# Kernel tuning notes

Hardware: AMD Instinct MI355X
Metric: run time of the kernel (lower is better)

## Reference

```python
import jax, jax.numpy as jnp
import numpy as np

L, N, C = 8192, 8, 3
DIM, DIM_OUT, K, RATIO = 64, 128, 16, 0.25
L2 = int(L * RATIO)  # 2048; note L % L2 == 0 (needed for the fmod quirk)
EPS = 1e-5


def layer_norm(x, g, b):
    m = jnp.mean(x, axis=-1, keepdims=True)
    v = jnp.mean(jnp.square(x - m), axis=-1, keepdims=True)  # biased var, as torch LayerNorm
    return (x - m) * jax.lax.rsqrt(v + EPS) * g + b


def mlp(x, w1, g1, b1, w2, g2, b2):
    h = x @ w1.T
    h = layer_norm(h, g1, b1)
    h = h @ w2.T
    h = layer_norm(h, g2, b2)
    return jax.nn.relu(h)


def setup_inputs() -> dict:
    key = jax.random.key(0)
    ks = jax.random.split(key, 5)
    coords = jax.random.normal(ks[0], (L, N, C), jnp.float32)
    features = jax.random.normal(ks[1], (L, N, DIM), jnp.float32)
    s1 = 1.0 / np.sqrt(DIM)
    s2 = 1.0 / np.sqrt(DIM_OUT)
    w1 = jax.random.uniform(ks[2], (DIM_OUT, DIM), jnp.float32, -s1, s1)
    w2 = jax.random.uniform(ks[3], (DIM_OUT, DIM_OUT), jnp.float32, -s2, s2)
    g1 = jnp.ones((DIM_OUT,), jnp.float32)
    b1 = jnp.zeros((DIM_OUT,), jnp.float32)
    g2 = jnp.ones((DIM_OUT,), jnp.float32)
    b2 = jnp.zeros((DIM_OUT,), jnp.float32)
    # RandomDecimate: random permutation of point indices, keep first L2 (same across batch)
    keep_idx = jax.random.permutation(ks[4], L)[:L2].astype(jnp.int32)
    return dict(coords=coords, features=features, w1=w1, g1=g1, b1=b1,
                w2=w2, g2=g2, b2=b2, keep_idx=keep_idx)


def reference(coords, features, w1, g1, b1, w2, g2, b2, keep_idx):
    # MLP on all points: [L, N, DIM_OUT]
    feats = mlp(features, w1, g1, b1, w2, g2, b2)
    # decimation: keep_coords [L2, N, C]
    keep_coords = coords[keep_idx]
    # per-batch KNN of kept points against all points
    c = coords.transpose(1, 0, 2)        # [N, L, C]
    kc = keep_coords.transpose(1, 0, 2)  # [N, L2, C]
    d2 = (jnp.sum(kc * kc, -1)[:, :, None]
          + jnp.sum(c * c, -1)[:, None, :]
          - 2.0 * jnp.einsum('nic,njc->nij', kc, c))  # [N, L2, L]
    _, nn_idx = jax.lax.top_k(-d2, K)    # [N, L2, K] indices into [0, L)
    # faithful to clusters.fmod_(L2) on flattened idx n*L+l (L % L2 == 0 => l % L2)
    nn_idx = nn_idx % L2
    # fused gather + amax pooling over K neighbors
    fT = feats.transpose(1, 0, 2)  # [N, L, DIM_OUT]
    gathered = jax.vmap(lambda f, idx: f[idx])(fT, nn_idx)  # [N, L2, K, DIM_OUT]
    pool_features = jnp.max(gathered, axis=2).transpose(1, 0, 2)  # [L2, N, DIM_OUT]
    return keep_coords, pool_features
```

## Files before the change

kernel.cpp:

```cpp
#include <hip/hip_runtime.h>
#include <stdint.h>

#define L_    8192
#define N_    8
#define L2_   2048
#define K_    16

typedef unsigned int uint;
typedef unsigned short ushort;
typedef unsigned long long u64;
typedef __attribute__((ext_vector_type(8))) short bh8;
typedef __attribute__((ext_vector_type(4))) float f32x4;

__device__ __forceinline__ ushort f2b(float f){
  uint u = __float_as_uint(f);
  return (ushort)((u + 0x7FFFu + ((u >> 16) & 1u)) >> 16);
}
__device__ __forceinline__ uint ford(float f){
  uint u = __float_as_uint(f);
  return u ^ ((uint)((int)u >> 31) | 0x80000000u);
}
__device__ __forceinline__ float unford(uint u){
  uint v = (u & 0x80000000u) ? (u ^ 0x80000000u) : ~u;
  return __uint_as_float(v);
}

__device__ __forceinline__ void ld8(float* t, const float* p){
  float4 a = *(const float4*)p; float4 b = *(const float4*)(p + 4);
  t[0]=a.x; t[1]=a.y; t[2]=a.z; t[3]=a.w; t[4]=b.x; t[5]=b.y; t[6]=b.z; t[7]=b.w;
}
__device__ __forceinline__ bh8 pack8(const float* v){
  bh8 r;
  #pragma unroll
  for (int j = 0; j < 8; ++j) r[j] = (short)f2b(v[j]);
  return r;
}

__global__ __launch_bounds__(256) void prep_pack_k(const float* __restrict__ coords,
                                                   const int* __restrict__ keep,
                                                   const float* __restrict__ w1,
                                                   const float* __restrict__ w2,
                                                   float* __restrict__ out0,
                                                   ushort* __restrict__ pw1,
                                                   ushort* __restrict__ pw2,
                                                   float4* __restrict__ sCF,
                                                   uint* __restrict__ oIdx,
                                                   uint* __restrict__ sPos,
                                                   float4* __restrict__ cBB){
  int blk = blockIdx.x;
  int tid = threadIdx.x;
  if (blk < 96){
    int e = blk * 256 + tid;
    if (e < 8192) pw1[e] = f2b(w1[e]);
    else          pw2[e - 8192] = f2b(w2[e - 8192]);
    return;
  }
  if (blk < 288){
    int t = (blk - 96) * 256 + tid;
    int i = t / 24; int rem = t - i * 24;
    out0[t] = coords[(size_t)keep[i] * 24 + rem];
    return;
  }
  int n = blk - 288;
  __shared__ uint hist[4096];
  __shared__ uint wsum[4];
  int lane = tid & 63, wv = tid >> 6;
  for (int i = tid; i < 4096; i += 256) hist[i] = 0;
  __syncthreads();
  for (int t = tid; t < 8192; t += 256){
    const float* cr = coords + ((size_t)t * 8 + n) * 3;
    float x = cr[0], y = cr[1], z = cr[2];
    int ix = (int)floorf((x + 4.f) * 2.f); ix = ix < 0 ? 0 : (ix > 15 ? 15 : ix);
    int iy = (int)floorf((y + 4.f) * 2.f); iy = iy < 0 ? 0 : (iy > 15 ? 15 : iy);
    int iz = (int)floorf((z + 4.f) * 2.f); iz = iz < 0 ? 0 : (iz > 15 ? 15 : iz);
    atomicAdd(&hist[(ix << 8) | (iy << 4) | iz], 1u);
  }
  __syncthreads();
  uint tt = 0;
  #pragma unroll
  for (int j = 0; j < 16; ++j) tt += hist[tid * 16 + j];
  uint sc = tt;
  #pragma unroll
  for (int m = 1; m < 64; m <<= 1){
    uint o = __shfl_up(sc, m, 64);
    if (lane >= m) sc += o;
  }
  if (lane == 63) wsum[wv] = sc;
  __syncthreads();
  uint wbase = 0;
  for (int w = 0; w < wv; ++w) wbase += wsum[w];
  uint run = wbase + sc - tt;
  #pragma unroll
  for (int j = 0; j < 16; ++j){
    uint v = hist[tid * 16 + j];
    hist[tid * 16 + j] = run;
    run += v;
  }
  __syncthreads();
  for (int t = tid; t < 8192; t += 256){
    const float* cr = coords + ((size_t)t * 8 + n) * 3;
    float x = cr[0], y = cr[1], z = cr[2];
    float cc;
    {
      #pragma clang fp contract(off)
      cc = x*x + y*y + z*z;
    }
    int ix = (int)floorf((x + 4.f) * 2.f); ix = ix < 0 ? 0 : (ix > 15 ? 15 : ix);
    int iy = (int)floorf((y + 4.f) * 2.f); iy = iy < 0 ? 0 : (iy > 15 ? 15 : iy);
    int iz = (int)floorf((z + 4.f) * 2.f); iz = iz < 0 ? 0 : (iz > 15 ? 15 : iz);
    uint pos = atomicAdd(&hist[(ix << 8) | (iy << 4) | iz], 1u);
    sCF[(n << 13) + pos] = make_float4(x, y, z, cc);
    oIdx[(n << 13) + pos] = (uint)t;
    sPos[(n << 13) + t]   = pos;
  }
  __syncthreads();
  if (tid < 128){
    float4 mn = make_float4(3.4e38f, 3.4e38f, 3.4e38f, 0.f);
    float4 mx = make_float4(-3.4e38f, -3.4e38f, -3.4e38f, 0.f);
    for (int j = 0; j < 64; ++j){
      float4 p = sCF[(n << 13) + tid * 64 + j];
      mn.x = fminf(mn.x, p.x); mn.y = fminf(mn.y, p.y); mn.z = fminf(mn.z, p.z);
      mx.x = fmaxf(mx.x, p.x); mx.y = fmaxf(mx.y, p.y); mx.z = fmaxf(mx.z, p.z);
    }
    cBB[(n << 8) + tid * 2]     = mn;
    cBB[(n << 8) + tid * 2 + 1] = mx;
  }
}

__global__ __launch_bounds__(256) void mlp_k(const float* __restrict__ feat,
                                             const ushort* __restrict__ pw1,
                                             const float* __restrict__ g1,
                                             const float* __restrict__ b1,
                                             const ushort* __restrict__ pw2,
                                             const float* __restrict__ g2,
                                             const float* __restrict__ b2,
                                             uint* __restrict__ fBw){
  __shared__ ushort hlds[16 * 136];
  __shared__ float pm1[4][16], pv1[4][16], pm2[4][16], pv2[4][16];
  int tid = threadIdx.x;
  int lane = tid & 63;
  int h = __builtin_amdgcn_readfirstlane(tid >> 6);
  int quad = lane >> 4, c = lane & 15;
  int rowg = blockIdx.x * 16;

  bh8 a1[2];
  {
    int rg = rowg + c; int l = rg & 2047, nb = rg >> 11;
    const float* xr = feat + (size_t)((l << 3) + nb) * 64 + quad * 8;
    float t0[8];
    ld8(t0, xr);      a1[0] = pack8(t0);
    ld8(t0, xr + 32); a1[1] = pack8(t0);
  }

  f32x4 acc1[2];
  acc1[0] = (f32x4){0.f,0.f,0.f,0.f}; acc1[1] = (f32x4){0.f,0.f,0.f,0.f};
  #pragma unroll
  for (int s = 0; s < 2; ++s){
    #pragma unroll
    for (int t = 0; t < 2; ++t){
      bh8 wb = *(const bh8*)(pw1 + (size_t)(h * 32 + t * 16 + c) * 64 + s * 32 + quad * 8);
      acc1[t] = __builtin_amdgcn_mfma_f32_16x16x32_bf16(a1[s], wb, acc1[t], 0, 0, 0);
    }
  }

  #pragma unroll
  for (int r = 0; r < 4; ++r){
    float s = acc1[0][r] + acc1[1][r];
    #pragma unroll
    for (int m = 1; m < 16; m <<= 1) s += __shfl_xor(s, m, 16);
    if (c == 0) pm1[h][quad * 4 + r] = s;
  }
  __syncthreads();
  float mean1[4], rstd1[4];
  #pragma unroll
  for (int r = 0; r < 4; ++r){
    int row = quad * 4 + r;
    mean1[r] = (pm1[0][row] + pm1[1][row] + pm1[2][row] + pm1[3][row]) * 0.0078125f;
  }
  #pragma unroll
  for (int r = 0; r < 4; ++r){
    float d0 = acc1[0][r] - mean1[r], d1 = acc1[1][r] - mean1[r];
    float s = d0 * d0 + d1 * d1;
    #pragma unroll
    for (int m = 1; m < 16; m <<= 1) s += __shfl_xor(s, m, 16);
    if (c == 0) pv1[h][quad * 4 + r] = s;
  }
  __syncthreads();
  #pragma unroll
  for (int r = 0; r < 4; ++r){
    int row = quad * 4 + r;
    rstd1[r] = rsqrtf((pv1[0][row] + pv1[1][row] + pv1[2][row] + pv1[3][row]) * 0.0078125f + 1e-5f);
  }
  #pragma unroll
  for (int t = 0; t < 2; ++t){
    int col = h * 32 + t * 16 + c;
    float gv = g1[col], bv = b1[col];
    #pragma unroll
    for (int r = 0; r < 4; ++r){
      float v = (acc1[t][r] - mean1[r]) * rstd1[r] * gv + bv;
      hlds[(quad * 4 + r) * 136 + col] = f2b(v);
    }
  }
  __syncthreads();

  f32x4 acc2[2];
  acc2[0] = (f32x4){0.f,0.f,0.f,0.f}; acc2[1] = (f32x4){0.f,0.f,0.f,0.f};
  #pragma unroll
  for (int s = 0; s < 4; ++s){
    bh8 af = *(const bh8*)(hlds + c * 136 + s * 32 + quad * 8);
    #pragma unroll
    for (int t = 0; t < 2; ++t){
      bh8 wb = *(const bh8*)(pw2 + (size_t)(h * 32 + t * 16 + c) * 128 + s * 32 + quad * 8);
      acc2[t] = __builtin_amdgcn_mfma_f32_16x16x32_bf16(af, wb, acc2[t], 0, 0, 0);
    }
  }

  #pragma unroll
  for (int r = 0; r < 4; ++r){
    float s = acc2[0][r] + acc2[1][r];
    #pragma unroll
    for (int m = 1; m < 16; m <<= 1) s += __shfl_xor(s, m, 16);
    if (c == 0) pm2[h][quad * 4 + r] = s;
  }
  __syncthreads();
  float mean2[4], rstd2[4];
  #pragma unroll
  for (int r = 0; r < 4; ++r){
    int row = quad * 4 + r;
    mean2[r] = (pm2[0][row] + pm2[1][row] + pm2[2][row] + pm2[3][row]) * 0.0078125f;
  }
  #pragma unroll
  for (int r = 0; r < 4; ++r){
    float d0 = acc2[0][r] - mean2[r], d1 = acc2[1][r] - mean2[r];
    float s = d0 * d0 + d1 * d1;
    #pragma unroll
    for (int m = 1; m < 16; m <<= 1) s += __shfl_xor(s, m, 16);
    if (c == 0) pv2[h][quad * 4 + r] = s;
  }
  __syncthreads();
  #pragma unroll
  for (int r = 0; r < 4; ++r){
    int row = quad * 4 + r;
    rstd2[r] = rsqrtf((pv2[0][row] + pv2[1][row] + pv2[2][row] + pv2[3][row]) * 0.0078125f + 1e-5f);
  }
  #pragma unroll
  for (int t = 0; t < 2; ++t){
    int col = h * 32 + t * 16 + c;
    float gv = g2[col], bv = b2[col];
    #pragma unroll
    for (int r = 0; r < 4; ++r){
      float v = fmaxf((acc2[t][r] - mean2[r]) * rstd2[r] * gv + bv, 0.f);
      hlds[(quad * 4 + r) * 136 + col] = f2b(v);
    }
  }
  __syncthreads();

  {
    int row16 = tid >> 4, pos = (tid & 15) * 4;
    const uint* src = (const uint*)hlds + row16 * 68 + pos;
    uint* dst = fBw + (size_t)(rowg + row16) * 64 + pos;
    *(uint4*)dst = *(const uint4*)src;
  }
}

__device__ __forceinline__ u64 shfl64(u64 v, int src){
  int lo = __shfl((int)(uint)v, src, 64);
  int hi = __shfl((int)(uint)(v >> 32), src, 64);
  return ((u64)(uint)hi << 32) | (uint)lo;
}

__device__ __forceinline__ u64 bsort64(u64 key, int lane){
  #pragma unroll
  for (int k = 2; k <= 64; k <<= 1){
    #pragma unroll
    for (int j = k >> 1; j > 0; j >>= 1){
      u64 o = shfl64(key, lane ^ j);
      bool lower = (lane & j) == 0;
      bool down  = (lane & k) == 0;
      bool takeMin = (lower == down);
      bool oLess = o < key;
      key = (oLess == takeMin) ? o : key;
    }
  }
  return key;
}
__device__ __forceinline__ u64 bmerge64(u64 key, int lane){
  #pragma unroll
  for (int j = 32; j > 0; j >>= 1){
    u64 o = shfl64(key, lane ^ j);
    bool lower = (lane & j) == 0;
    bool oLess = o < key;
    key = (oLess == lower) ? o : key;
  }
  return key;
}

__device__ __attribute__((noinline)) u64 drainx(u64* ldsq, int qcount, int lane){
  u64 a = (lane < qcount) ? ldsq[lane] : ~0ull;
  a = bsort64(a, lane);
  if (qcount > 64){
    u64 b = (64 + lane < qcount) ? ldsq[64 + lane] : ~0ull;
    b = bsort64(b, lane);
    u64 br = shfl64(b, 63 - lane);
    a = a < br ? a : br;
    a = bmerge64(a, lane);
  }
  if (lane < 16) ldsq[lane] = a;
  return a;
}

__device__ __forceinline__ void updq(u64* ql, int& qc, int& nx, float& thr,
                                     float qw, int lane){
  int q = qc;
  u64 k0 = (lane < q) ? ql[lane] : ~0ull;
  u64 k1 = (64 + lane < q) ? ql[64 + lane] : ~0ull;
  uint h0 = (uint)(k0 >> 32), h1 = (uint)(k1 >> 32);
  uint m = h0 < h1 ? h0 : h1;
  uint v = 0u;
  #pragma unroll
  for (int b = 31; b >= 16; --b){
    uint tv = v | (1u << b);
    if (__popcll(__ballot(m < tv)) < 16) v = tv;
  }
  uint vb = (v >= 0xFFFF0000u) ? 0xFFFFFFFFu : (v + 0x10000u);

  bool kp0 = (h0 <= vb);
  u64 bal0 = __ballot(kp0);
  int r0 = __builtin_amdgcn_mbcnt_lo((uint)bal0, 0);
  r0 = __builtin_amdgcn_mbcnt_hi((uint)(bal0 >> 32), r0);
  if (kp0) ql[r0] = k0;
  int c0 = __popcll(bal0);
  bool kp1 = (h1 <= vb);
  u64 bal1 = __ballot(kp1);
  int r1 = __builtin_amdgcn_mbcnt_lo((uint)bal1, 0);
  r1 = __builtin_amdgcn_mbcnt_hi((uint)(bal1 >> 32), r1);
  if (kp1) ql[c0 + r1] = k1;
  int out = c0 + __popcll(bal1);

  uint hb = vb;
  if (out > 31){
    u64 a = drainx(ql, out, lane);
    hb = (uint)(shfl64(a, 15) >> 32);
    out = 16;
  }
  qc = out;
  nx = out + 33;
  thr = unford(hb) + 1e-3f - qw;
}

__global__ __launch_bounds__(256) void knn_pool_k(const float4* __restrict__ sCF,
                                                  const uint* __restrict__ oIdx,
                                                  const uint* __restrict__ sPos,
                                                  const float4* __restrict__ cBB,
                                                  const int* __restrict__ keep,
                                                  const uint* __restrict__ fB32,
                                                  float* __restrict__ out1){
  __shared__ u64 q8[4][2][128];
  int tid = threadIdx.x, lane = tid & 63;
  int wv = tid >> 6;
  int g0 = blockIdx.x * 8 + wv * 2;
  int n = g0 >> 11;
  int i0 = g0 & 2047;
  const float4* base = sCF + (n << 13);
  const uint* oix = oIdx + (n << 13);
  const float4* bb = cBB + (n << 8);

  u64 res[2];
  #pragma unroll
  for (int qi = 0; qi < 2; ++qi){
    int iq = i0 + qi;
    uint pos = sPos[(n << 13) + keep[iq]];
    float4 qv = base[pos];
    int cs = (int)(pos >> 6);
    float qw = qv.w;
    float q2x = -2.f * qv.x, q2y = -2.f * qv.y, q2z = -2.f * qv.z;

    float lb0, lb1;
    {
      float4 mn = bb[lane * 2], mx = bb[lane * 2 + 1];
      float dx = fmaxf(fmaxf(mn.x - qv.x, qv.x - mx.x), 0.f);
      float dy = fmaxf(fmaxf(mn.y - qv.y, qv.y - mx.y), 0.f);
      float dz = fmaxf(fmaxf(mn.z - qv.z, qv.z - mx.z), 0.f);
      lb0 = __builtin_fmaf(dx, dx, __builtin_fmaf(dy, dy, dz * dz));
      mn = bb[(lane + 64) * 2]; mx = bb[(lane + 64) * 2 + 1];
      dx = fmaxf(fmaxf(mn.x - qv.x, qv.x - mx.x), 0.f);
      dy = fmaxf(fmaxf(mn.y - qv.y, qv.y - mx.y), 0.f);
      dz = fmaxf(fmaxf(mn.z - qv.z, qv.z - mx.z), 0.f);
      lb1 = __builtin_fmaf(dx, dx, __builtin_fmaf(dy, dy, dz * dz));
    }

    float thr = 3.4e38f, d2thr = 3.4e38f;
    int qc = 0, nx = 49;
    u64* ql = q8[wv][qi];

    for (int ii = 0; ii < 128; ++ii){
      int c = (cs + ii) & 127;
      float lbc = __shfl((c & 64) ? lb1 : lb0, c & 63, 64);
      if (lbc > d2thr) continue;
      int j = (c << 6) + lane;
      float4 cf = base[j];
      float s = __builtin_fmaf(q2x, cf.x, __builtin_fmaf(q2y, cf.y,
                __builtin_fmaf(q2z, cf.z, cf.w)));
      u64 bal = __ballot(s <= thr);
      if (bal){
        if (s <= thr){
          float d2;
          {
            #pragma clang fp contract(off)
            float dot = qv.x*cf.x + qv.y*cf.y + qv.z*cf.z;
            d2 = (qw + cf.w) - 2.0f * dot;
          }
          uint oj = oix[j];
          int rel = __builtin_amdgcn_mbcnt_lo((uint)bal, 0);
          rel = __builtin_amdgcn_mbcnt_hi((uint)(bal >> 32), rel);
          ql[qc + rel] = ((u64)ford(d2) << 32) | oj;
        }
        qc += __popcll(bal);
        if (qc >= nx){
          updq(ql, qc, nx, thr, qw, lane);
          d2thr = thr + qw;
        }
      }
    }
    res[qi] = drainx(ql, qc, lane);
  }

  const uint* frow = fB32 + ((size_t)(n << 11) << 6);
  float a0 = -3.4e38f, a1v = -3.4e38f, b0 = -3.4e38f, b1v = -3.4e38f;
  #pragma unroll
  for (int k = 0; k < 16; ++k){
    int idxA = (int)(shfl64(res[0], k) & 2047u);
    int idxB = (int)(shfl64(res[1], k) & 2047u);
    uint uA = frow[((size_t)idxA << 6) + lane];
    uint uB = frow[((size_t)idxB << 6) + lane];
    a0  = fmaxf(a0,  __uint_as_float((uA & 0xFFFFu) << 16));
    a1v = fmaxf(a1v, __uint_as_float((uA >> 16) << 16));
    b0  = fmaxf(b0,  __uint_as_float((uB & 0xFFFFu) << 16));
    b1v = fmaxf(b1v, __uint_as_float((uB >> 16) << 16));
  }
  float2* oA = (float2*)(out1 + (size_t)(i0 * 8 + n) * 128);
  float2* oB = (float2*)(out1 + (size_t)((i0 + 1) * 8 + n) * 128);
  oA[lane] = make_float2(a0, a1v);
  oB[lane] = make_float2(b0, b1v);
}

extern "C" void kernel_launch(void* const* d_in, const int* in_sizes, int n_in,
                              void* d_out, int out_size, void* d_ws, size_t ws_size,
                              hipStream_t stream){
  const float* coords = (const float*)d_in[0];
  const float* feat   = (const float*)d_in[1];
  const float* w1     = (const float*)d_in[2];
  const float* g1     = (const float*)d_in[3];
  const float* b1     = (const float*)d_in[4];
  const float* w2     = (const float*)d_in[5];
  const float* g2     = (const float*)d_in[6];
  const float* b2     = (const float*)d_in[7];
  const int*   keep   = (const int*)d_in[8];
  float* out0 = (float*)d_out;
  float* out1 = out0 + 49152;

  char* ws = (char*)d_ws;
  uint*   fB   = (uint*)ws;
  ushort* pw1  = (ushort*)(ws + (4 << 20));
  ushort* pw2  = pw1 + 8192;
  float4* sCF  = (float4*)(ws + (4 << 20) + (64 << 10));
  uint*   oIdx = (uint*)(ws + (5 << 20) + (64 << 10));
  uint*   sPos = oIdx + 65536;
  float4* cBB  = (float4*)(ws + (5 << 20) + (576 << 10));

  hipLaunchKernelGGL(prep_pack_k, dim3(296), dim3(256), 0, stream,
                     coords, keep, w1, w2, out0, pw1, pw2, sCF, oIdx, sPos, cBB);
  hipLaunchKernelGGL(mlp_k, dim3(1024), dim3(256), 0, stream,
                     feat, pw1, g1, b1, pw2, g2, b2, fB);
  hipLaunchKernelGGL(knn_pool_k, dim3(2048), dim3(256), 0, stream,
                     sCF, oIdx, sPos, cBB, keep, fB, out1);
}
```

Before: 185.0 us.

## Morton-order grid cells, split sort kernel, and prune KNN chunks via ballot mask

Points are now ordered by a Morton (Z-order) code of the 16^3 grid cell instead of raster order, which tightens the per-chunk bounding boxes. The per-point preprocessing is spread across many blocks and a separate 8-block sort kernel builds the histogram and scatter. The KNN loop visits the home chunk first, then builds a ballot mask of only the chunks whose bounding box passes the threshold and walks it with software prefetch. The cost is an extra launch, extra workspace traffic, and a candidate mask that is fixed after the first chunk rather than re-tightened as the threshold shrinks.

```diff
diff --git a/kernel.cpp b/kernel.cpp
--- a/kernel.cpp
+++ b/kernel.cpp
@@ -36,94 +36,115 @@
   return r;
 }
 
+__device__ __forceinline__ uint sp4(uint v){
+  return (v & 1u) | ((v & 2u) << 2) | ((v & 4u) << 4) | ((v & 8u) << 6);
+}
+__device__ __forceinline__ int cell16(float x){
+  int i = (int)floorf((x + 4.f) * 2.f);
+  return i < 0 ? 0 : (i > 15 ? 15 : i);
+}
+
 __global__ __launch_bounds__(256) void prep_pack_k(const float* __restrict__ coords,
                                                    const int* __restrict__ keep,
                                                    const float* __restrict__ w1,
                                                    const float* __restrict__ w2,
+                                                   float4* __restrict__ cF,
+                                                   uint* __restrict__ cellId,
                                                    float* __restrict__ out0,
                                                    ushort* __restrict__ pw1,
-                                                   ushort* __restrict__ pw2,
-                                                   float4* __restrict__ sCF,
-                                                   uint* __restrict__ oIdx,
-                                                   uint* __restrict__ sPos,
-                                                   float4* __restrict__ cBB){
+                                                   ushort* __restrict__ pw2){
   int blk = blockIdx.x;
   int tid = threadIdx.x;
   if (blk < 96){
     int e = blk * 256 + tid;
     if (e < 8192) pw1[e] = f2b(w1[e]);
     else          pw2[e - 8192] = f2b(w2[e - 8192]);
-    return;
-  }
-  if (blk < 288){
-    int t = (blk - 96) * 256 + tid;
-    int i = t / 24; int rem = t - i * 24;
-    out0[t] = coords[(size_t)keep[i] * 24 + rem];
-    return;
-  }
-  int n = blk - 288;
-  __shared__ uint hist[4096];
-  __shared__ uint wsum[4];
-  int lane = tid & 63, wv = tid >> 6;
-  for (int i = tid; i < 4096; i += 256) hist[i] = 0;
-  __syncthreads();
-  for (int t = tid; t < 8192; t += 256){
-    const float* cr = coords + ((size_t)t * 8 + n) * 3;
-    float x = cr[0], y = cr[1], z = cr[2];
-    int ix = (int)floorf((x + 4.f) * 2.f); ix = ix < 0 ? 0 : (ix > 15 ? 15 : ix);
-    int iy = (int)floorf((y + 4.f) * 2.f); iy = iy < 0 ? 0 : (iy > 15 ? 15 : iy);
-    int iz = (int)floorf((z + 4.f) * 2.f); iz = iz < 0 ? 0 : (iz > 15 ? 15 : iz);
-    atomicAdd(&hist[(ix << 8) | (iy << 4) | iz], 1u);
-  }
-  __syncthreads();
-  uint tt = 0;
-  #pragma unroll
-  for (int j = 0; j < 16; ++j) tt += hist[tid * 16 + j];
-  uint sc = tt;
-  #pragma unroll
-  for (int m = 1; m < 64; m <<= 1){
-    uint o = __shfl_up(sc, m, 64);
-    if (lane >= m) sc += o;
-  }
-  if (lane == 63) wsum[wv] = sc;
-  __syncthreads();
-  uint wbase = 0;
-  for (int w = 0; w < wv; ++w) wbase += wsum[w];
-  uint run = wbase + sc - tt;
-  #pragma unroll
-  for (int j = 0; j < 16; ++j){
-    uint v = hist[tid * 16 + j];
-    hist[tid * 16 + j] = run;
-    run += v;
-  }
-  __syncthreads();
-  for (int t = tid; t < 8192; t += 256){
-    const float* cr = coords + ((size_t)t * 8 + n) * 3;
+  } else if (blk < 352){
+    int e = (blk - 96) * 256 + tid;
+    int l = e >> 3, n = e & 7;
+    const float* cr = coords + (size_t)e * 3;
     float x = cr[0], y = cr[1], z = cr[2];
     float cc;
     {
       #pragma clang fp contract(off)
       cc = x*x + y*y + z*z;
     }
-    int ix = (int)floorf((x + 4.f) * 2.f); ix = ix < 0 ? 0 : (ix > 15 ? 15 : ix);
-    int iy = (int)floorf((y + 4.f) * 2.f); iy = iy < 0 ? 0 : (iy > 15 ? 15 : iy);
-    int iz = (int)floorf((z + 4.f) * 2.f); iz = iz < 0 ? 0 : (iz > 15 ? 15 : iz);
-    uint pos = atomicAdd(&hist[(ix << 8) | (iy << 4) | iz], 1u);
-    sCF[(n << 13) + pos] = make_float4(x, y, z, cc);
+    cF[(n << 13) + l] = make_float4(x, y, z, cc);
+    uint mort = (sp4((uint)cell16(x)) << 2) | (sp4((uint)cell16(y)) << 1)
+              | sp4((uint)cell16(z));
+    cellId[(n << 13) + l] = mort;
+  } else {
+    int t = (blk - 352) * 256 + tid;
+    int i = t / 24; int rem = t - i * 24;
+    out0[t] = coords[(size_t)keep[i] * 24 + rem];
+  }
+}
+
+__global__ __launch_bounds__(256) void sort_k(const float4* __restrict__ cF,
+                                              const uint* __restrict__ cellId,
+                                              float4* __restrict__ sCF,
+                                              uint* __restrict__ oIdx,
+                                              uint* __restrict__ sPos,
+                                              float4* __restrict__ cBB){
+  __shared__ uint hist[4096];
+  __shared__ uint wsum[4];
+  int n = blockIdx.x;
+  int tid = threadIdx.x, lane = tid & 63, wv = tid >> 6;
+  const uint* cid = cellId + (n << 13);
+  const float4* cf = cF + (n << 13);
+
+  for (int i = tid; i < 4096; i += 256) hist[i] = 0;
+  __syncthreads();
+  for (int t = tid; t < 8192; t += 256)
+    atomicAdd(&hist[cid[t]], 1u);
+  __syncthreads();
+  uint tt = 0;
+  #pragma unroll
+  for (int j = 0; j < 16; ++j) tt += hist[tid * 16 + j];
+  uint sc = tt;
+  #pragma unroll
+  for (int m = 1; m < 64; m <<= 1){
+    uint o = __shfl_up(sc, m, 64);
+    if (lane >= m) sc += o;
+  }
+  if (lane == 63) wsum[wv] = sc;
+  __syncthreads();
+  uint wbase = 0;
+  for (int w = 0; w < wv; ++w) wbase += wsum[w];
+  uint run = wbase + sc - tt;
+  #pragma unroll
+  for (int j = 0; j < 16; ++j){
+    uint v = hist[tid * 16 + j];
+    hist[tid * 16 + j] = run;
+    run += v;
+  }
+  __syncthreads();
+  for (int t = tid; t < 8192; t += 256){
+    uint pos = atomicAdd(&hist[cid[t]], 1u);
+    sCF[(n << 13) + pos] = cf[t];
     oIdx[(n << 13) + pos] = (uint)t;
     sPos[(n << 13) + t]   = pos;
   }
   __syncthreads();
-  if (tid < 128){
+  {
+    int ch = tid >> 1, half = tid & 1;
     float4 mn = make_float4(3.4e38f, 3.4e38f, 3.4e38f, 0.f);
     float4 mx = make_float4(-3.4e38f, -3.4e38f, -3.4e38f, 0.f);
-    for (int j = 0; j < 64; ++j){
-      float4 p = sCF[(n << 13) + tid * 64 + j];
+    for (int j = half * 32; j < half * 32 + 32; ++j){
+      float4 p = sCF[(n << 13) + ch * 64 + j];
       mn.x = fminf(mn.x, p.x); mn.y = fminf(mn.y, p.y); mn.z = fminf(mn.z, p.z);
       mx.x = fmaxf(mx.x, p.x); mx.y = fmaxf(mx.y, p.y); mx.z = fmaxf(mx.z, p.z);
     }
-    cBB[(n << 8) + tid * 2]     = mn;
-    cBB[(n << 8) + tid * 2 + 1] = mx;
+    mn.x = fminf(mn.x, __shfl_xor(mn.x, 1, 64));
+    mn.y = fminf(mn.y, __shfl_xor(mn.y, 1, 64));
+    mn.z = fminf(mn.z, __shfl_xor(mn.z, 1, 64));
+    mx.x = fmaxf(mx.x, __shfl_xor(mx.x, 1, 64));
+    mx.y = fmaxf(mx.y, __shfl_xor(mx.y, 1, 64));
+    mx.z = fmaxf(mx.z, __shfl_xor(mx.z, 1, 64));
+    if (half == 0){
+      cBB[(n << 8) + ch * 2]     = mn;
+      cBB[(n << 8) + ch * 2 + 1] = mx;
+    }
   }
 }
 
@@ -346,6 +367,12 @@
   qc = out;
   nx = out + 33;
   thr = unford(hb) + 1e-3f - qw;
+}
+
+__device__ __forceinline__ int nextbit(u64& m0, u64& m1){
+  if (m0){ int b = __builtin_ctzll(m0); m0 &= m0 - 1; return b; }
+  if (m1){ int b = __builtin_ctzll(m1); m1 &= m1 - 1; return b + 64; }
+  return -1;
 }
 
 __global__ __launch_bounds__(256) void knn_pool_k(const float4* __restrict__ sCF,
@@ -389,39 +416,55 @@
       lb1 = __builtin_fmaf(dx, dx, __builtin_fmaf(dy, dy, dz * dz));
     }
 
-    float thr = 3.4e38f, d2thr = 3.4e38f;
+    float thr = 3.4e38f;
     int qc = 0, nx = 49;
     u64* ql = q8[wv][qi];
 
-    for (int ii = 0; ii < 128; ++ii){
-      int c = (cs + ii) & 127;
-      float lbc = __shfl((c & 64) ? lb1 : lb0, c & 63, 64);
-      if (lbc > d2thr) continue;
-      int j = (c << 6) + lane;
-      float4 cf = base[j];
-      float s = __builtin_fmaf(q2x, cf.x, __builtin_fmaf(q2y, cf.y,
-                __builtin_fmaf(q2z, cf.z, cf.w)));
-      u64 bal = __ballot(s <= thr);
-      if (bal){
-        if (s <= thr){
-          float d2;
-          {
-            #pragma clang fp contract(off)
-            float dot = qv.x*cf.x + qv.y*cf.y + qv.z*cf.z;
-            d2 = (qw + cf.w) - 2.0f * dot;
-          }
-          uint oj = oix[j];
-          int rel = __builtin_amdgcn_mbcnt_lo((uint)bal, 0);
-          rel = __builtin_amdgcn_mbcnt_hi((uint)(bal >> 32), rel);
-          ql[qc + rel] = ((u64)ford(d2) << 32) | oj;
-        }
-        qc += __popcll(bal);
-        if (qc >= nx){
-          updq(ql, qc, nx, thr, qw, lane);
-          d2thr = thr + qw;
-        }
-      }
-    }
+    #define PROCC(cf, c) { \
+      float s = __builtin_fmaf(q2x, (cf).x, __builtin_fmaf(q2y, (cf).y, \
+                __builtin_fmaf(q2z, (cf).z, (cf).w))); \
+      u64 bal = __ballot(s <= thr); \
+      if (bal){ \
+        if (s <= thr){ \
+          float d2; \
+          { \
+            _Pragma("clang fp contract(off)") \
+            float dot = qv.x*(cf).x + qv.y*(cf).y + qv.z*(cf).z; \
+            d2 = (qw + (cf).w) - 2.0f * dot; \
+          } \
+          uint oj = oix[((c) << 6) + lane]; \
+          int rel = __builtin_amdgcn_mbcnt_lo((uint)bal, 0); \
+          rel = __builtin_amdgcn_mbcnt_hi((uint)(bal >> 32), rel); \
+          ql[qc + rel] = ((u64)ford(d2) << 32) | oj; \
+        } \
+        qc += __popcll(bal); \
+        if (qc >= nx) updq(ql, qc, nx, thr, qw, lane); \
+      } \
+    }
+
+    {
+      float4 cf = base[(cs << 6) + lane];
+      PROCC(cf, cs);
+    }
+    float d2thr = thr + qw;
+
+    u64 m0 = __ballot(lb0 <= d2thr);
+    u64 m1 = __ballot(lb1 <= d2thr);
+    if (cs < 64) m0 &= ~(1ull << cs);
+    else         m1 &= ~(1ull << (cs - 64));
+
+    int c = nextbit(m0, m1);
+    float4 cf;
+    if (c >= 0) cf = base[(c << 6) + lane];
+    while (c >= 0){
+      int c2 = nextbit(m0, m1);
+      float4 cf2;
+      if (c2 >= 0) cf2 = base[(c2 << 6) + lane];
+      PROCC(cf, c);
+      c = c2; cf = cf2;
+    }
+    #undef PROCC
+
     res[qi] = drainx(ql, qc, lane);
   }
 
@@ -460,16 +503,20 @@
   float* out1 = out0 + 49152;
 
   char* ws = (char*)d_ws;
-  uint*   fB   = (uint*)ws;
-  ushort* pw1  = (ushort*)(ws + (4 << 20));
-  ushort* pw2  = pw1 + 8192;
-  float4* sCF  = (float4*)(ws + (4 << 20) + (64 << 10));
-  uint*   oIdx = (uint*)(ws + (5 << 20) + (64 << 10));
-  uint*   sPos = oIdx + 65536;
-  float4* cBB  = (float4*)(ws + (5 << 20) + (576 << 10));
-
-  hipLaunchKernelGGL(prep_pack_k, dim3(296), dim3(256), 0, stream,
-                     coords, keep, w1, w2, out0, pw1, pw2, sCF, oIdx, sPos, cBB);
+  float4* cF     = (float4*)ws;
+  uint*   cellId = (uint*)(ws + (1 << 20));
+  uint*   fB     = (uint*)ws;
+  float4* sCF    = (float4*)(ws + (4 << 20));
+  uint*   oIdx   = (uint*)(ws + (5 << 20));
+  uint*   sPos   = oIdx + 65536;
+  float4* cBB    = (float4*)(ws + (5 << 20) + (512 << 10));
+  ushort* pw1    = (ushort*)(ws + (6 << 20));
+  ushort* pw2    = pw1 + 8192;
+
+  hipLaunchKernelGGL(prep_pack_k, dim3(544), dim3(256), 0, stream,
+                     coords, keep, w1, w2, cF, cellId, out0, pw1, pw2);
+  hipLaunchKernelGGL(sort_k, dim3(8), dim3(256), 0, stream,
+                     cF, cellId, sCF, oIdx, sPos, cBB);
   hipLaunchKernelGGL(mlp_k, dim3(1024), dim3(256), 0, stream,
                      feat, pw1, g1, b1, pw2, g2, b2, fB);
   hipLaunchKernelGGL(knn_pool_k, dim3(2048), dim3(256), 0, stream,
```

Result: slower. 230.6 us (+24.6%).

## Split grid binning into parallel prep and Morton-ordered counting sort kernel

Applied to the files above, without the earlier changes.

Cell id computation and coord packing move into a wide, fully parallel prep stage. The per-batch counting sort becomes a separate kernel that reads the precomputed cell ids and builds chunk bounding boxes with shared-memory atomics. Cells are now numbered in Morton (Z-order) rather than row-major order, so the 64-point chunks become more spatially compact and their bounding boxes tighter for KNN pruning. The cost is an extra kernel launch and an intermediate buffer (cF and cellId) that shares workspace with fB.

```diff
diff --git a/kernel.cpp b/kernel.cpp
--- a/kernel.cpp
+++ b/kernel.cpp
@@ -36,94 +36,111 @@
   return r;
 }
 
+__device__ __forceinline__ uint sp4(uint v){
+  return (v & 1u) | ((v & 2u) << 2) | ((v & 4u) << 4) | ((v & 8u) << 6);
+}
+__device__ __forceinline__ int cell16(float x){
+  int i = (int)floorf((x + 4.f) * 2.f);
+  return i < 0 ? 0 : (i > 15 ? 15 : i);
+}
+
 __global__ __launch_bounds__(256) void prep_pack_k(const float* __restrict__ coords,
                                                    const int* __restrict__ keep,
                                                    const float* __restrict__ w1,
                                                    const float* __restrict__ w2,
+                                                   float4* __restrict__ cF,
+                                                   uint* __restrict__ cellId,
                                                    float* __restrict__ out0,
                                                    ushort* __restrict__ pw1,
-                                                   ushort* __restrict__ pw2,
-                                                   float4* __restrict__ sCF,
-                                                   uint* __restrict__ oIdx,
-                                                   uint* __restrict__ sPos,
-                                                   float4* __restrict__ cBB){
+                                                   ushort* __restrict__ pw2){
   int blk = blockIdx.x;
   int tid = threadIdx.x;
   if (blk < 96){
     int e = blk * 256 + tid;
     if (e < 8192) pw1[e] = f2b(w1[e]);
     else          pw2[e - 8192] = f2b(w2[e - 8192]);
-    return;
-  }
-  if (blk < 288){
-    int t = (blk - 96) * 256 + tid;
-    int i = t / 24; int rem = t - i * 24;
-    out0[t] = coords[(size_t)keep[i] * 24 + rem];
-    return;
-  }
-  int n = blk - 288;
-  __shared__ uint hist[4096];
-  __shared__ uint wsum[4];
-  int lane = tid & 63, wv = tid >> 6;
-  for (int i = tid; i < 4096; i += 256) hist[i] = 0;
-  __syncthreads();
-  for (int t = tid; t < 8192; t += 256){
-    const float* cr = coords + ((size_t)t * 8 + n) * 3;
-    float x = cr[0], y = cr[1], z = cr[2];
-    int ix = (int)floorf((x + 4.f) * 2.f); ix = ix < 0 ? 0 : (ix > 15 ? 15 : ix);
-    int iy = (int)floorf((y + 4.f) * 2.f); iy = iy < 0 ? 0 : (iy > 15 ? 15 : iy);
-    int iz = (int)floorf((z + 4.f) * 2.f); iz = iz < 0 ? 0 : (iz > 15 ? 15 : iz);
-    atomicAdd(&hist[(ix << 8) | (iy << 4) | iz], 1u);
-  }
-  __syncthreads();
-  uint tt = 0;
-  #pragma unroll
-  for (int j = 0; j < 16; ++j) tt += hist[tid * 16 + j];
-  uint sc = tt;
-  #pragma unroll
-  for (int m = 1; m < 64; m <<= 1){
-    uint o = __shfl_up(sc, m, 64);
-    if (lane >= m) sc += o;
-  }
-  if (lane == 63) wsum[wv] = sc;
-  __syncthreads();
-  uint wbase = 0;
-  for (int w = 0; w < wv; ++w) wbase += wsum[w];
-  uint run = wbase + sc - tt;
-  #pragma unroll
-  for (int j = 0; j < 16; ++j){
-    uint v = hist[tid * 16 + j];
-    hist[tid * 16 + j] = run;
-    run += v;
-  }
-  __syncthreads();
-  for (int t = tid; t < 8192; t += 256){
-    const float* cr = coords + ((size_t)t * 8 + n) * 3;
+  } else if (blk < 352){
+    int e = (blk - 96) * 256 + tid;
+    int l = e >> 3, n = e & 7;
+    const float* cr = coords + (size_t)e * 3;
     float x = cr[0], y = cr[1], z = cr[2];
     float cc;
     {
       #pragma clang fp contract(off)
       cc = x*x + y*y + z*z;
     }
-    int ix = (int)floorf((x + 4.f) * 2.f); ix = ix < 0 ? 0 : (ix > 15 ? 15 : ix);
-    int iy = (int)floorf((y + 4.f) * 2.f); iy = iy < 0 ? 0 : (iy > 15 ? 15 : iy);
-    int iz = (int)floorf((z + 4.f) * 2.f); iz = iz < 0 ? 0 : (iz > 15 ? 15 : iz);
-    uint pos = atomicAdd(&hist[(ix << 8) | (iy << 4) | iz], 1u);
-    sCF[(n << 13) + pos] = make_float4(x, y, z, cc);
+    cF[(n << 13) + l] = make_float4(x, y, z, cc);
+    uint mort = (sp4((uint)cell16(x)) << 2) | (sp4((uint)cell16(y)) << 1)
+              | sp4((uint)cell16(z));
+    cellId[(n << 13) + l] = mort;
+  } else {
+    int t = (blk - 352) * 256 + tid;
+    int i = t / 24; int rem = t - i * 24;
+    out0[t] = coords[(size_t)keep[i] * 24 + rem];
+  }
+}
+
+__global__ __launch_bounds__(256) void sort_k(const float4* __restrict__ cF,
+                                              const uint* __restrict__ cellId,
+                                              float4* __restrict__ sCF,
+                                              uint* __restrict__ oIdx,
+                                              uint* __restrict__ sPos,
+                                              float4* __restrict__ cBB){
+  __shared__ uint hist[4096];
+  __shared__ uint wsum[4];
+  __shared__ uint bmn[128][3], bmx[128][3];
+  int n = blockIdx.x;
+  int tid = threadIdx.x, lane = tid & 63, wv = tid >> 6;
+  const uint* cid = cellId + (n << 13);
+  const float4* cf = cF + (n << 13);
+
+  for (int i = tid; i < 4096; i += 256) hist[i] = 0;
+  if (tid < 128){
+    bmn[tid][0] = bmn[tid][1] = bmn[tid][2] = 0xFFFFFFFFu;
+    bmx[tid][0] = bmx[tid][1] = bmx[tid][2] = 0u;
+  }
+  __syncthreads();
+  for (int t = tid; t < 8192; t += 256)
+    atomicAdd(&hist[cid[t]], 1u);
+  __syncthreads();
+  uint tt = 0;
+  #pragma unroll
+  for (int j = 0; j < 16; ++j) tt += hist[tid * 16 + j];
+  uint sc = tt;
+  #pragma unroll
+  for (int m = 1; m < 64; m <<= 1){
+    uint o = __shfl_up(sc, m, 64);
+    if (lane >= m) sc += o;
+  }
+  if (lane == 63) wsum[wv] = sc;
+  __syncthreads();
+  uint wbase = 0;
+  for (int w = 0; w < wv; ++w) wbase += wsum[w];
+  uint run = wbase + sc - tt;
+  #pragma unroll
+  for (int j = 0; j < 16; ++j){
+    uint v = hist[tid * 16 + j];
+    hist[tid * 16 + j] = run;
+    run += v;
+  }
+  __syncthreads();
+  for (int t = tid; t < 8192; t += 256){
+    float4 p = cf[t];
+    uint pos = atomicAdd(&hist[cid[t]], 1u);
+    sCF[(n << 13) + pos] = p;
     oIdx[(n << 13) + pos] = (uint)t;
     sPos[(n << 13) + t]   = pos;
+    int ch = (int)(pos >> 6);
+    atomicMin(&bmn[ch][0], ford(p.x)); atomicMax(&bmx[ch][0], ford(p.x));
+    atomicMin(&bmn[ch][1], ford(p.y)); atomicMax(&bmx[ch][1], ford(p.y));
+    atomicMin(&bmn[ch][2], ford(p.z)); atomicMax(&bmx[ch][2], ford(p.z));
   }
   __syncthreads();
   if (tid < 128){
-    float4 mn = make_float4(3.4e38f, 3.4e38f, 3.4e38f, 0.f);
-    float4 mx = make_float4(-3.4e38f, -3.4e38f, -3.4e38f, 0.f);
-    for (int j = 0; j < 64; ++j){
-      float4 p = sCF[(n << 13) + tid * 64 + j];
-      mn.x = fminf(mn.x, p.x); mn.y = fminf(mn.y, p.y); mn.z = fminf(mn.z, p.z);
-      mx.x = fmaxf(mx.x, p.x); mx.y = fmaxf(mx.y, p.y); mx.z = fmaxf(mx.z, p.z);
-    }
-    cBB[(n << 8) + tid * 2]     = mn;
-    cBB[(n << 8) + tid * 2 + 1] = mx;
+    cBB[(n << 8) + tid * 2] = make_float4(unford(bmn[tid][0]), unford(bmn[tid][1]),
+                                          unford(bmn[tid][2]), 0.f);
+    cBB[(n << 8) + tid * 2 + 1] = make_float4(unford(bmx[tid][0]), unford(bmx[tid][1]),
+                                              unford(bmx[tid][2]), 0.f);
   }
 }
 
@@ -460,16 +477,20 @@
   float* out1 = out0 + 49152;
 
   char* ws = (char*)d_ws;
-  uint*   fB   = (uint*)ws;
-  ushort* pw1  = (ushort*)(ws + (4 << 20));
-  ushort* pw2  = pw1 + 8192;
-  float4* sCF  = (float4*)(ws + (4 << 20) + (64 << 10));
-  uint*   oIdx = (uint*)(ws + (5 << 20) + (64 << 10));
-  uint*   sPos = oIdx + 65536;
-  float4* cBB  = (float4*)(ws + (5 << 20) + (576 << 10));
-
-  hipLaunchKernelGGL(prep_pack_k, dim3(296), dim3(256), 0, stream,
-                     coords, keep, w1, w2, out0, pw1, pw2, sCF, oIdx, sPos, cBB);
+  float4* cF     = (float4*)ws;
+  uint*   cellId = (uint*)(ws + (1 << 20));
+  uint*   fB     = (uint*)ws;
+  float4* sCF    = (float4*)(ws + (4 << 20));
+  uint*   oIdx   = (uint*)(ws + (5 << 20));
+  uint*   sPos   = oIdx + 65536;
+  float4* cBB    = (float4*)(ws + (5 << 20) + (512 << 10));
+  ushort* pw1    = (ushort*)(ws + (6 << 20));
+  ushort* pw2    = pw1 + 8192;
+
+  hipLaunchKernelGGL(prep_pack_k, dim3(544), dim3(256), 0, stream,
+                     coords, keep, w1, w2, cF, cellId, out0, pw1, pw2);
+  hipLaunchKernelGGL(sort_k, dim3(8), dim3(256), 0, stream,
+                     cF, cellId, sCF, oIdx, sPos, cBB);
   hipLaunchKernelGGL(mlp_k, dim3(1024), dim3(256), 0, stream,
                      feat, pw1, g1, b1, pw2, g2, b2, fB);
   hipLaunchKernelGGL(knn_pool_k, dim3(2048), dim3(256), 0, stream,
```

Result: no change. 182.4 us (-1.4%).
